# Optimization experiments

Measured on AMD Instinct MI355X. Metric: run time of the kernel, lower is better.

The kernel has to match this reference:

```python
import jax, jax.numpy as jnp
import numpy as np

NUM_CLASSES = 81
NEG_POS_RATIO = 3  # neg_pos init arg
POS_FRAC = 0.02    # realistic fraction of matched (positive) priors


def setup_inputs() -> dict:
    key = jax.random.key(0)
    k1, k2, k3, k4, k5 = jax.random.split(key, 5)
    B, P, C = 32, 24564, NUM_CLASSES
    loc_data = jax.random.normal(k1, (B, P, 4), jnp.float32)
    conf_data = jax.random.normal(k2, (B, P, C), jnp.float32)
    loc_targets = jax.random.normal(k3, (B, P, 4), jnp.float32)
    raw_labels = jax.random.randint(k4, (B, P), 1, C)
    is_pos = jax.random.uniform(k5, (B, P)) < POS_FRAC
    conf_targets = jnp.where(is_pos, raw_labels, 0).astype(jnp.int32)
    return {"loc_data": loc_data, "conf_data": conf_data,
            "loc_targets": loc_targets, "conf_targets": conf_targets}


def _smooth_l1(x):
    ax = jnp.abs(x)
    return jnp.where(ax < 1.0, 0.5 * x * x, ax - 0.5)


def reference(loc_data, conf_data, loc_targets, conf_targets):
    # loc_data [B,P,4], conf_data [B,P,C], conf_targets [B,P] int
    B, P, C = conf_data.shape
    pos = conf_targets > 0  # [B,P]

    # localization smooth-L1 over positive priors only (sum reduction)
    loc_loss = jnp.sum(_smooth_l1(loc_data - loc_targets) * pos[..., None].astype(loc_data.dtype))

    # per-prior CE loss: logsumexp - logit[target]
    lse = jax.nn.logsumexp(conf_data, axis=-1)  # [B,P]
    tgt_logit = jnp.take_along_axis(conf_data, conf_targets[..., None].astype(jnp.int32), axis=-1)[..., 0]
    ce = lse - tgt_logit  # [B,P]

    # hard negative mining: zero out positives, sort descending, pick pivot at 3*num_pos
    mined = jnp.where(pos, 0.0, ce)
    sorted_desc = jnp.flip(jnp.sort(mined, axis=1), axis=1)  # [B,P]
    num_pos = jnp.sum(pos, axis=1)  # [B]
    num_neg = jnp.clip(NEG_POS_RATIO * num_pos, 0, P - 1)
    pivot = jnp.take_along_axis(sorted_desc, num_neg[:, None], axis=1)  # [B,1]
    neg = mined > pivot

    sel = (pos | neg).astype(ce.dtype)
    conf_loss = jnp.sum(ce * sel)

    n_matched = jnp.maximum(jnp.sum(num_pos), 1).astype(conf_data.dtype)
    return (loc_loss + conf_loss) / n_matched
```

## Files before the change

kernel.cpp:

```cpp
#include <hip/hip_runtime.h>
#include <cmath>
#include <cstdint>

#define NB 32
#define NP 24564
#define NC 81
#define NEG_POS 3

static constexpr size_t MINED_ELEMS = (size_t)NB * NP;
static constexpr size_t MINED_BYTES = MINED_ELEMS * sizeof(float);

#define NTILES4 ((int)(MINED_ELEMS / 4))
#define MAIN_BLOCKS 2047
#define TOTAL_WAVES (MAIN_BLOCKS * 4)
#define ITERS 24


__device__ __forceinline__ float wave_reduce_sum(float v) {
#pragma unroll
  for (int off = 32; off > 0; off >>= 1) v += __shfl_down(v, off, 64);
  return v;
}

__device__ __forceinline__ float smooth_l1_4(float4 a, float4 t) {
  float acc = 0.f, d, ax;
  d = a.x - t.x; ax = fabsf(d); acc += (ax < 1.f) ? 0.5f * d * d : ax - 0.5f;
  d = a.y - t.y; ax = fabsf(d); acc += (ax < 1.f) ? 0.5f * d * d : ax - 0.5f;
  d = a.z - t.z; ax = fabsf(d); acc += (ax < 1.f) ? 0.5f * d * d : ax - 0.5f;
  d = a.w - t.w; ax = fabsf(d); acc += (ax < 1.f) ? 0.5f * d * d : ax - 0.5f;
  return acc;
}

__global__ void mb_init(double* __restrict__ acc, int* __restrict__ num_pos) {
  int t = threadIdx.x;
  if (t < 3) acc[t] = 0.0;
  if (t < NB) num_pos[t] = 0;
}

__global__ __launch_bounds__(256, 8) void mb_main(
    const float* __restrict__ conf_data, const int* __restrict__ conf_targets,
    float* __restrict__ mined) {
  __shared__ float lds[4][332];

  const int tid  = (int)threadIdx.x;
  const int wid  = tid >> 6, lane = tid & 63;
  const int r    = lane >> 4, il = lane & 15;
  float* __restrict__ L = lds[wid];

  const int l17   = (lane < 17) ? lane : 16;
  const int ldst1 = (lane < 17) ? (256 + 4 * l17) : 328;

  int tile = (int)blockIdx.x * 4 + wid;
  float4 c0, c1;
  {
    const float4* __restrict__ src =
        reinterpret_cast<const float4*>(conf_data) + (size_t)tile * 81;
    c0 = src[lane];
    c1 = src[64 + l17];
  }

#pragma unroll 1
  for (int k = 0; k < ITERS; ++k) {
    *reinterpret_cast<float4*>(&L[4 * lane]) = c0;
    *reinterpret_cast<float4*>(&L[ldst1]) = c1;

    {
      int nt = tile + TOTAL_WAVES;
      nt = (nt < NTILES4) ? nt : tile;
      const float4* __restrict__ src =
          reinterpret_cast<const float4*>(conf_data) + (size_t)nt * 81;
      c0 = src[lane];
      c1 = src[64 + l17];
    }
    __builtin_amdgcn_sched_barrier(0);

    const int4 tg = *reinterpret_cast<const int4*>(conf_targets + (size_t)tile * 4);
    const int tgt = (r == 0) ? tg.x : (r == 1) ? tg.y : (r == 2) ? tg.z : tg.w;

    const int rb = 81 * r;
    float e = __expf(L[rb + il]) + __expf(L[rb + il + 16]) +
              __expf(L[rb + il + 32]) + __expf(L[rb + il + 48]) +
              __expf(L[rb + il + 64]);
    if (il == 0) e += __expf(L[rb + 80]);
    e += __shfl_xor(e, 1, 64);
    e += __shfl_xor(e, 2, 64);
    e += __shfl_xor(e, 4, 64);
    e += __shfl_xor(e, 8, 64);

    const float tv = L[rb + tgt];
    const float ce = __logf(e) - tv;
    const float val = (tgt > 0) ? -ce : ce;
    mined[tile * 4 + r] = val;

    tile += TOTAL_WAVES;
  }
}

__global__ __launch_bounds__(1024) void mb_select(
    const float* __restrict__ mined, const float* __restrict__ loc_data,
    const float* __restrict__ loc_targets, double* __restrict__ acc,
    int* __restrict__ num_pos) {
  const int b = blockIdx.x;
  const float* __restrict__ row = mined + (size_t)b * NP;
  const int tid = threadIdx.x;
  const int wid = tid >> 6;
  const int lane = tid & 63;

  __shared__ int hist[16][256];
  __shared__ int total[256];
  __shared__ int suffix[256];
  __shared__ unsigned s_prefix;
  __shared__ int s_k;
  __shared__ int s_np;

  {
    int np = 0;
    float cp = 0.f, lv = 0.f;
    for (int q = tid; q < NP / 4; q += 1024) {
      const float4 v = reinterpret_cast<const float4*>(row)[q];
      const float vv[4] = {v.x, v.y, v.z, v.w};
#pragma unroll
      for (int j = 0; j < 4; ++j) {
        if (__float_as_uint(vv[j]) >> 31) {
          np++;
          cp += -vv[j];
          const size_t flat = (size_t)b * NP + 4 * q + j;
          lv += smooth_l1_4(
              *reinterpret_cast<const float4*>(loc_data + flat * 4),
              *reinterpret_cast<const float4*>(loc_targets + flat * 4));
        }
      }
    }
    __shared__ float rednp[16], redcp[16], redlv[16];
    float wnp = wave_reduce_sum((float)np);
    float wcp = wave_reduce_sum(cp);
    float wlv = wave_reduce_sum(lv);
    if (lane == 0) { rednp[wid] = wnp; redcp[wid] = wcp; redlv[wid] = wlv; }
    __syncthreads();
    if (tid == 0) {
      float tnp = 0.f, tcp = 0.f, tlv = 0.f;
#pragma unroll
      for (int i = 0; i < 16; ++i) { tnp += rednp[i]; tcp += redcp[i]; tlv += redlv[i]; }
      const int npi = (int)tnp;
      s_np = npi;
      num_pos[b] = npi;
      if (tcp != 0.f) atomicAdd(&acc[1], (double)tcp);
      if (tlv != 0.f) atomicAdd(&acc[0], (double)tlv);
      int k = NEG_POS * npi;
      if (k > NP - 1) k = NP - 1;
      s_k = k;
      s_prefix = 0u;
    }
    __syncthreads();
  }

  for (int shift = 24; shift >= 0; shift -= 8) {
    for (int i = tid; i < 16 * 256; i += 1024) ((int*)hist)[i] = 0;
    __syncthreads();
    const unsigned mask = (shift == 24) ? 0u : (0xFFFFFFFFu << (shift + 8));
    const unsigned pfx = s_prefix;
    const int kcur = s_k;

    for (int q = tid; q < NP / 4; q += 1024) {
      const float4 v = reinterpret_cast<const float4*>(row)[q];
      unsigned u;
      u = __float_as_uint(v.x); u = (u >> 31) ? 0u : u; if ((u & mask) == pfx) atomicAdd(&hist[wid][(u >> shift) & 255], 1);
      u = __float_as_uint(v.y); u = (u >> 31) ? 0u : u; if ((u & mask) == pfx) atomicAdd(&hist[wid][(u >> shift) & 255], 1);
      u = __float_as_uint(v.z); u = (u >> 31) ? 0u : u; if ((u & mask) == pfx) atomicAdd(&hist[wid][(u >> shift) & 255], 1);
      u = __float_as_uint(v.w); u = (u >> 31) ? 0u : u; if ((u & mask) == pfx) atomicAdd(&hist[wid][(u >> shift) & 255], 1);
    }
    __syncthreads();

    if (tid < 256) {
      int t = 0;
#pragma unroll
      for (int w = 0; w < 16; ++w) t += hist[w][tid];
      total[tid] = t;
    }
    __syncthreads();

    if (wid == 0) {
      const int t0_ = total[4 * lane + 0];
      const int t1_ = total[4 * lane + 1];
      const int t2_ = total[4 * lane + 2];
      const int t3_ = total[4 * lane + 3];
      const int s3 = t3_;
      const int s2 = t2_ + s3;
      const int s1 = t1_ + s2;
      const int s0 = t0_ + s1;
      int acc_ = s0;
#pragma unroll
      for (int off = 1; off < 64; off <<= 1) {
        const int o = __shfl_down(acc_, off, 64);
        if (lane + off < 64) acc_ += o;
      }
      const int excl = acc_ - s0;
      suffix[4 * lane + 0] = s0 + excl;
      suffix[4 * lane + 1] = s1 + excl;
      suffix[4 * lane + 2] = s2 + excl;
      suffix[4 * lane + 3] = s3 + excl;
    }
    __syncthreads();

    if (tid < 256) {
      const int cs = suffix[tid] - total[tid];
      if (kcur >= cs && kcur < cs + total[tid]) {
        s_prefix = pfx | ((unsigned)tid << shift);
        s_k = kcur - cs;
      }
    }
    __syncthreads();
  }

  const unsigned vbits = s_prefix;
  float sum = 0.f;
  for (int q = tid; q < NP / 4; q += 1024) {
    const float4 v = reinterpret_cast<const float4*>(row)[q];
    unsigned u;
    u = __float_as_uint(v.x); u = (u >> 31) ? 0u : u; if (u > vbits) sum += v.x;
    u = __float_as_uint(v.y); u = (u >> 31) ? 0u : u; if (u > vbits) sum += v.y;
    u = __float_as_uint(v.z); u = (u >> 31) ? 0u : u; if (u > vbits) sum += v.z;
    u = __float_as_uint(v.w); u = (u >> 31) ? 0u : u; if (u > vbits) sum += v.w;
  }

  __shared__ float wsum[16];
  float w = wave_reduce_sum(sum);
  if (lane == 0) wsum[wid] = w;
  __syncthreads();
  if (tid == 0) {
    float t = 0.f;
#pragma unroll
    for (int i = 0; i < 16; ++i) t += wsum[i];
    atomicAdd(&acc[2], (double)t);
  }
}

__global__ void mb_finalize(const double* __restrict__ acc,
                            const int* __restrict__ num_pos,
                            float* __restrict__ out) {
  if (threadIdx.x == 0) {
    int tot = 0;
#pragma unroll
    for (int i = 0; i < NB; ++i) tot += num_pos[i];
    const double n = (double)(tot > 0 ? tot : 1);
    out[0] = (float)((acc[0] + acc[1] + acc[2]) / n);
  }
}

extern "C" void kernel_launch(void* const* d_in, const int* in_sizes, int n_in,
                              void* d_out, int out_size, void* d_ws, size_t ws_size,
                              hipStream_t stream) {
  const float* loc_data     = (const float*)d_in[0];
  const float* conf_data    = (const float*)d_in[1];
  const float* loc_targets  = (const float*)d_in[2];
  const int*   conf_targets = (const int*)d_in[3];
  float* out = (float*)d_out;

  float*  mined   = (float*)d_ws;
  double* acc     = (double*)((char*)d_ws + MINED_BYTES);
  int*    num_pos = (int*)((char*)d_ws + MINED_BYTES + 3 * sizeof(double));

  mb_init<<<1, 64, 0, stream>>>(acc, num_pos);

  mb_main<<<MAIN_BLOCKS, 256, 0, stream>>>(conf_data, conf_targets, mined);

  mb_select<<<NB, 1024, 0, stream>>>(mined, loc_data, loc_targets, acc, num_pos);

  mb_finalize<<<1, 64, 0, stream>>>(acc, num_pos, out);
}
```

Measured before the change: 103.6 us.

## Fuse radix-select sum pass into histogram passes, double-buffer main loads, drop init kernel

mb_select now builds the first radix histogram during the positive-count/loc-loss pass and keeps per-bucket float sums, so the sum of negatives above the pivot comes out of the suffix scans. This removes one full histogram pass and the final summation pass over each row. mb_main gets a two-deep register double buffer for conf_data and target loads, which raises memory-level parallelism at some register cost. Per-batch partials are written instead of double atomics, so the mb_init launch is gone. The float LDS atomics and float accumulation order may shift numerics slightly.

```diff
diff --git a/kernel.cpp b/kernel.cpp
--- a/kernel.cpp
+++ b/kernel.cpp
@@ -13,7 +13,7 @@
 #define NTILES4 ((int)(MINED_ELEMS / 4))
 #define MAIN_BLOCKS 2047
 #define TOTAL_WAVES (MAIN_BLOCKS * 4)
-#define ITERS 24
+#define KITERS 12
 
 
 __device__ __forceinline__ float wave_reduce_sum(float v) {
@@ -31,12 +31,6 @@
   return acc;
 }
 
-__global__ void mb_init(double* __restrict__ acc, int* __restrict__ num_pos) {
-  int t = threadIdx.x;
-  if (t < 3) acc[t] = 0.0;
-  if (t < NB) num_pos[t] = 0;
-}
-
 __global__ __launch_bounds__(256, 8) void mb_main(
     const float* __restrict__ conf_data, const int* __restrict__ conf_targets,
     float* __restrict__ mined) {
@@ -50,55 +44,85 @@
   const int l17   = (lane < 17) ? lane : 16;
   const int ldst1 = (lane < 17) ? (256 + 4 * l17) : 328;
 
+#define LOAD_DATA(c0, c1, t)                                            \
+  do {                                                                  \
+    const float4* __restrict__ _s =                                     \
+        reinterpret_cast<const float4*>(conf_data) + (size_t)(t) * 81;  \
+    (c0) = _s[lane];                                                    \
+    (c1) = _s[64 + l17];                                                \
+  } while (0)
+
+#define STAGE(c0, c1)                                     \
+  do {                                                    \
+    *reinterpret_cast<float4*>(&L[4 * lane]) = (c0);      \
+    *reinterpret_cast<float4*>(&L[ldst1]) = (c1);         \
+  } while (0)
+
+#define COMPUTE(t, tg)                                                        \
+  do {                                                                        \
+    const int tgt = (r == 0) ? (tg).x : (r == 1) ? (tg).y                     \
+                  : (r == 2) ? (tg).z : (tg).w;                               \
+    const int rb = 81 * r;                                                    \
+    float e = __expf(L[rb + il]) + __expf(L[rb + il + 16]) +                  \
+              __expf(L[rb + il + 32]) + __expf(L[rb + il + 48]) +             \
+              __expf(L[rb + il + 64]);                                        \
+    if (il == 0) e += __expf(L[rb + 80]);                                     \
+    e += __shfl_xor(e, 1, 64);                                                \
+    e += __shfl_xor(e, 2, 64);                                                \
+    e += __shfl_xor(e, 4, 64);                                                \
+    e += __shfl_xor(e, 8, 64);                                                \
+    const float tv = L[rb + tgt];                                             \
+    const float ce = __logf(e) - tv;                                          \
+    const float val = (tgt > 0) ? -ce : ce;                                   \
+    mined[(t) * 4 + r] = val;                                                 \
+  } while (0)
+
   int tile = (int)blockIdx.x * 4 + wid;
-  float4 c0, c1;
+  float4 a0, a1, b0, b1;
+  int4 tgA, tgB, tgN;
+
+  LOAD_DATA(a0, a1, tile);
+  tgA = *reinterpret_cast<const int4*>(conf_targets + (size_t)tile * 4);
   {
-    const float4* __restrict__ src =
-        reinterpret_cast<const float4*>(conf_data) + (size_t)tile * 81;
-    c0 = src[lane];
-    c1 = src[64 + l17];
+    const int tB = tile + TOTAL_WAVES;
+    LOAD_DATA(b0, b1, tB);
+    tgB = *reinterpret_cast<const int4*>(conf_targets + (size_t)tB * 4);
   }
 
 #pragma unroll 1
-  for (int k = 0; k < ITERS; ++k) {
-    *reinterpret_cast<float4*>(&L[4 * lane]) = c0;
-    *reinterpret_cast<float4*>(&L[ldst1]) = c1;
-
+  for (int k = 0; k < KITERS; ++k) {
+    STAGE(a0, a1);
     {
-      int nt = tile + TOTAL_WAVES;
-      nt = (nt < NTILES4) ? nt : tile;
-      const float4* __restrict__ src =
-          reinterpret_cast<const float4*>(conf_data) + (size_t)nt * 81;
-      c0 = src[lane];
-      c1 = src[64 + l17];
+      int tn = tile + 2 * TOTAL_WAVES;
+      tn = (tn < NTILES4) ? tn : tile;
+      LOAD_DATA(a0, a1, tn);
+      tgN = *reinterpret_cast<const int4*>(conf_targets + (size_t)tn * 4);
     }
     __builtin_amdgcn_sched_barrier(0);
-
-    const int4 tg = *reinterpret_cast<const int4*>(conf_targets + (size_t)tile * 4);
-    const int tgt = (r == 0) ? tg.x : (r == 1) ? tg.y : (r == 2) ? tg.z : tg.w;
-
-    const int rb = 81 * r;
-    float e = __expf(L[rb + il]) + __expf(L[rb + il + 16]) +
-              __expf(L[rb + il + 32]) + __expf(L[rb + il + 48]) +
-              __expf(L[rb + il + 64]);
-    if (il == 0) e += __expf(L[rb + 80]);
-    e += __shfl_xor(e, 1, 64);
-    e += __shfl_xor(e, 2, 64);
-    e += __shfl_xor(e, 4, 64);
-    e += __shfl_xor(e, 8, 64);
-
-    const float tv = L[rb + tgt];
-    const float ce = __logf(e) - tv;
-    const float val = (tgt > 0) ? -ce : ce;
-    mined[tile * 4 + r] = val;
-
+    COMPUTE(tile, tgA);
+    tgA = tgN;
     tile += TOTAL_WAVES;
-  }
+
+    STAGE(b0, b1);
+    {
+      int tn = tile + 2 * TOTAL_WAVES;
+      tn = (tn < NTILES4) ? tn : tile;
+      LOAD_DATA(b0, b1, tn);
+      tgN = *reinterpret_cast<const int4*>(conf_targets + (size_t)tn * 4);
+    }
+    __builtin_amdgcn_sched_barrier(0);
+    COMPUTE(tile, tgB);
+    tgB = tgN;
+    tile += TOTAL_WAVES;
+  }
+#undef LOAD_DATA
+#undef STAGE
+#undef COMPUTE
 }
 
 __global__ __launch_bounds__(1024) void mb_select(
     const float* __restrict__ mined, const float* __restrict__ loc_data,
-    const float* __restrict__ loc_targets, double* __restrict__ acc,
+    const float* __restrict__ loc_targets, float* __restrict__ partial,
     int* __restrict__ num_pos) {
   const int b = blockIdx.x;
   const float* __restrict__ row = mined + (size_t)b * NP;
@@ -106,144 +130,153 @@
   const int wid = tid >> 6;
   const int lane = tid & 63;
 
-  __shared__ int hist[16][256];
-  __shared__ int total[256];
-  __shared__ int suffix[256];
+  __shared__ int   hist[16][256];
+  __shared__ float fsum[16][256];
+  __shared__ int   total[256];
+  __shared__ float ftotal[256];
+  __shared__ int   suffix[256];
+  __shared__ float fsuffix[256];
+  __shared__ float redf[3][16];
   __shared__ unsigned s_prefix;
   __shared__ int s_k;
-  __shared__ int s_np;
+  __shared__ float s_gsum, s_cp, s_lv;
+
+  if (tid == 0) { s_prefix = 0u; s_gsum = 0.f; }
+
+  for (int i = tid; i < 16 * 256; i += 1024) { ((int*)hist)[i] = 0; ((float*)fsum)[i] = 0.f; }
+  __syncthreads();
 
   {
-    int np = 0;
-    float cp = 0.f, lv = 0.f;
+    float np = 0.f, cp = 0.f, lv = 0.f;
     for (int q = tid; q < NP / 4; q += 1024) {
       const float4 v = reinterpret_cast<const float4*>(row)[q];
       const float vv[4] = {v.x, v.y, v.z, v.w};
 #pragma unroll
       for (int j = 0; j < 4; ++j) {
-        if (__float_as_uint(vv[j]) >> 31) {
-          np++;
+        unsigned u = __float_as_uint(vv[j]);
+        if (u >> 31) {
+          np += 1.f;
           cp += -vv[j];
           const size_t flat = (size_t)b * NP + 4 * q + j;
           lv += smooth_l1_4(
               *reinterpret_cast<const float4*>(loc_data + flat * 4),
               *reinterpret_cast<const float4*>(loc_targets + flat * 4));
+          u = 0u;
         }
+        atomicAdd(&hist[wid][u >> 24], 1);
+        atomicAdd(&fsum[wid][u >> 24], __uint_as_float(u));
       }
     }
-    __shared__ float rednp[16], redcp[16], redlv[16];
-    float wnp = wave_reduce_sum((float)np);
+    float wnp = wave_reduce_sum(np);
     float wcp = wave_reduce_sum(cp);
     float wlv = wave_reduce_sum(lv);
-    if (lane == 0) { rednp[wid] = wnp; redcp[wid] = wcp; redlv[wid] = wlv; }
+    if (lane == 0) { redf[0][wid] = wnp; redf[1][wid] = wcp; redf[2][wid] = wlv; }
+  }
+  __syncthreads();
+  if (tid == 0) {
+    float tnp = 0.f, tcp = 0.f, tlv = 0.f;
+#pragma unroll
+    for (int i = 0; i < 16; ++i) { tnp += redf[0][i]; tcp += redf[1][i]; tlv += redf[2][i]; }
+    const int npi = (int)tnp;
+    num_pos[b] = npi;
+    s_cp = tcp; s_lv = tlv;
+    int k = NEG_POS * npi;
+    if (k > NP - 1) k = NP - 1;
+    s_k = k;
+  }
+  __syncthreads();
+
+#define PASS_EPILOGUE(SHIFT)                                                  \
+  do {                                                                        \
+    if (tid < 256) {                                                          \
+      int t = 0; float f = 0.f;                                               \
+      _Pragma("unroll")                                                       \
+      for (int w = 0; w < 16; ++w) { t += hist[w][tid]; f += fsum[w][tid]; }  \
+      total[tid] = t; ftotal[tid] = f;                                        \
+    }                                                                         \
+    __syncthreads();                                                          \
+    if (wid == 0) {                                                           \
+      int t3 = total[4 * lane + 3], t2 = total[4 * lane + 2];                 \
+      int t1 = total[4 * lane + 1], t0 = total[4 * lane + 0];                 \
+      float f3 = ftotal[4 * lane + 3], f2 = ftotal[4 * lane + 2];             \
+      float f1 = ftotal[4 * lane + 1], f0 = ftotal[4 * lane + 0];             \
+      const int is3 = t3, is2 = t2 + is3, is1 = t1 + is2, is0 = t0 + is1;     \
+      const float fs3 = f3, fs2 = f2 + fs3, fs1 = f1 + fs2, fs0 = f0 + fs1;   \
+      int ia = is0; float fa = fs0;                                           \
+      _Pragma("unroll")                                                       \
+      for (int off = 1; off < 64; off <<= 1) {                                \
+        const int io = __shfl_down(ia, off, 64);                              \
+        const float fo = __shfl_down(fa, off, 64);                            \
+        if (lane + off < 64) { ia += io; fa += fo; }                          \
+      }                                                                       \
+      const int iex = ia - is0; const float fex = fa - fs0;                   \
+      suffix[4 * lane + 0] = is0 + iex; fsuffix[4 * lane + 0] = fs0 + fex;    \
+      suffix[4 * lane + 1] = is1 + iex; fsuffix[4 * lane + 1] = fs1 + fex;    \
+      suffix[4 * lane + 2] = is2 + iex; fsuffix[4 * lane + 2] = fs2 + fex;    \
+      suffix[4 * lane + 3] = is3 + iex; fsuffix[4 * lane + 3] = fs3 + fex;    \
+    }                                                                         \
+    __syncthreads();                                                          \
+    if (tid < 256) {                                                          \
+      const int kcur = s_k;                                                   \
+      const int cs = suffix[tid] - total[tid];                                \
+      if (kcur >= cs && kcur < cs + total[tid]) {                             \
+        s_prefix |= ((unsigned)tid << (SHIFT));                               \
+        s_k = kcur - cs;                                                      \
+        s_gsum += fsuffix[tid] - ftotal[tid];                                 \
+      }                                                                       \
+    }                                                                         \
+    __syncthreads();                                                          \
+  } while (0)
+
+  PASS_EPILOGUE(24);
+
+  for (int shift = 16; shift >= 0; shift -= 8) {
+    for (int i = tid; i < 16 * 256; i += 1024) { ((int*)hist)[i] = 0; ((float*)fsum)[i] = 0.f; }
     __syncthreads();
-    if (tid == 0) {
-      float tnp = 0.f, tcp = 0.f, tlv = 0.f;
-#pragma unroll
-      for (int i = 0; i < 16; ++i) { tnp += rednp[i]; tcp += redcp[i]; tlv += redlv[i]; }
-      const int npi = (int)tnp;
-      s_np = npi;
-      num_pos[b] = npi;
-      if (tcp != 0.f) atomicAdd(&acc[1], (double)tcp);
-      if (tlv != 0.f) atomicAdd(&acc[0], (double)tlv);
-      int k = NEG_POS * npi;
-      if (k > NP - 1) k = NP - 1;
-      s_k = k;
-      s_prefix = 0u;
-    }
-    __syncthreads();
-  }
-
-  for (int shift = 24; shift >= 0; shift -= 8) {
-    for (int i = tid; i < 16 * 256; i += 1024) ((int*)hist)[i] = 0;
-    __syncthreads();
-    const unsigned mask = (shift == 24) ? 0u : (0xFFFFFFFFu << (shift + 8));
+    const unsigned mask = 0xFFFFFFFFu << (shift + 8);
     const unsigned pfx = s_prefix;
-    const int kcur = s_k;
 
     for (int q = tid; q < NP / 4; q += 1024) {
       const float4 v = reinterpret_cast<const float4*>(row)[q];
       unsigned u;
-      u = __float_as_uint(v.x); u = (u >> 31) ? 0u : u; if ((u & mask) == pfx) atomicAdd(&hist[wid][(u >> shift) & 255], 1);
-      u = __float_as_uint(v.y); u = (u >> 31) ? 0u : u; if ((u & mask) == pfx) atomicAdd(&hist[wid][(u >> shift) & 255], 1);
-      u = __float_as_uint(v.z); u = (u >> 31) ? 0u : u; if ((u & mask) == pfx) atomicAdd(&hist[wid][(u >> shift) & 255], 1);
-      u = __float_as_uint(v.w); u = (u >> 31) ? 0u : u; if ((u & mask) == pfx) atomicAdd(&hist[wid][(u >> shift) & 255], 1);
+      u = __float_as_uint(v.x); u = (u >> 31) ? 0u : u;
+      if ((u & mask) == pfx) { atomicAdd(&hist[wid][(u >> shift) & 255], 1); atomicAdd(&fsum[wid][(u >> shift) & 255], __uint_as_float(u)); }
+      u = __float_as_uint(v.y); u = (u >> 31) ? 0u : u;
+      if ((u & mask) == pfx) { atomicAdd(&hist[wid][(u >> shift) & 255], 1); atomicAdd(&fsum[wid][(u >> shift) & 255], __uint_as_float(u)); }
+      u = __float_as_uint(v.z); u = (u >> 31) ? 0u : u;
+      if ((u & mask) == pfx) { atomicAdd(&hist[wid][(u >> shift) & 255], 1); atomicAdd(&fsum[wid][(u >> shift) & 255], __uint_as_float(u)); }
+      u = __float_as_uint(v.w); u = (u >> 31) ? 0u : u;
+      if ((u & mask) == pfx) { atomicAdd(&hist[wid][(u >> shift) & 255], 1); atomicAdd(&fsum[wid][(u >> shift) & 255], __uint_as_float(u)); }
     }
     __syncthreads();
 
-    if (tid < 256) {
-      int t = 0;
-#pragma unroll
-      for (int w = 0; w < 16; ++w) t += hist[w][tid];
-      total[tid] = t;
-    }
-    __syncthreads();
-
-    if (wid == 0) {
-      const int t0_ = total[4 * lane + 0];
-      const int t1_ = total[4 * lane + 1];
-      const int t2_ = total[4 * lane + 2];
-      const int t3_ = total[4 * lane + 3];
-      const int s3 = t3_;
-      const int s2 = t2_ + s3;
-      const int s1 = t1_ + s2;
-      const int s0 = t0_ + s1;
-      int acc_ = s0;
-#pragma unroll
-      for (int off = 1; off < 64; off <<= 1) {
-        const int o = __shfl_down(acc_, off, 64);
-        if (lane + off < 64) acc_ += o;
-      }
-      const int excl = acc_ - s0;
-      suffix[4 * lane + 0] = s0 + excl;
-      suffix[4 * lane + 1] = s1 + excl;
-      suffix[4 * lane + 2] = s2 + excl;
-      suffix[4 * lane + 3] = s3 + excl;
-    }
-    __syncthreads();
-
-    if (tid < 256) {
-      const int cs = suffix[tid] - total[tid];
-      if (kcur >= cs && kcur < cs + total[tid]) {
-        s_prefix = pfx | ((unsigned)tid << shift);
-        s_k = kcur - cs;
-      }
-    }
-    __syncthreads();
-  }
-
-  const unsigned vbits = s_prefix;
-  float sum = 0.f;
-  for (int q = tid; q < NP / 4; q += 1024) {
-    const float4 v = reinterpret_cast<const float4*>(row)[q];
-    unsigned u;
-    u = __float_as_uint(v.x); u = (u >> 31) ? 0u : u; if (u > vbits) sum += v.x;
-    u = __float_as_uint(v.y); u = (u >> 31) ? 0u : u; if (u > vbits) sum += v.y;
-    u = __float_as_uint(v.z); u = (u >> 31) ? 0u : u; if (u > vbits) sum += v.z;
-    u = __float_as_uint(v.w); u = (u >> 31) ? 0u : u; if (u > vbits) sum += v.w;
-  }
-
-  __shared__ float wsum[16];
-  float w = wave_reduce_sum(sum);
-  if (lane == 0) wsum[wid] = w;
-  __syncthreads();
+    if (shift == 16) PASS_EPILOGUE(16);
+    else if (shift == 8) PASS_EPILOGUE(8);
+    else PASS_EPILOGUE(0);
+  }
+#undef PASS_EPILOGUE
+
   if (tid == 0) {
-    float t = 0.f;
-#pragma unroll
-    for (int i = 0; i < 16; ++i) t += wsum[i];
-    atomicAdd(&acc[2], (double)t);
-  }
-}
-
-__global__ void mb_finalize(const double* __restrict__ acc,
+    partial[b * 4 + 0] = s_lv;
+    partial[b * 4 + 1] = s_cp;
+    partial[b * 4 + 2] = s_gsum;
+  }
+}
+
+__global__ void mb_finalize(const float* __restrict__ partial,
                             const int* __restrict__ num_pos,
                             float* __restrict__ out) {
   if (threadIdx.x == 0) {
+    double s = 0.0;
     int tot = 0;
 #pragma unroll
-    for (int i = 0; i < NB; ++i) tot += num_pos[i];
+    for (int i = 0; i < NB; ++i) {
+      s += (double)partial[i * 4 + 0] + (double)partial[i * 4 + 1] +
+           (double)partial[i * 4 + 2];
+      tot += num_pos[i];
+    }
     const double n = (double)(tot > 0 ? tot : 1);
-    out[0] = (float)((acc[0] + acc[1] + acc[2]) / n);
+    out[0] = (float)(s / n);
   }
 }
 
@@ -256,15 +289,13 @@
   const int*   conf_targets = (const int*)d_in[3];
   float* out = (float*)d_out;
 
-  float*  mined   = (float*)d_ws;
-  double* acc     = (double*)((char*)d_ws + MINED_BYTES);
-  int*    num_pos = (int*)((char*)d_ws + MINED_BYTES + 3 * sizeof(double));
-
-  mb_init<<<1, 64, 0, stream>>>(acc, num_pos);
+  float* mined   = (float*)d_ws;
+  float* partial = (float*)((char*)d_ws + MINED_BYTES);
+  int*   num_pos = (int*)((char*)d_ws + MINED_BYTES + 512);
 
   mb_main<<<MAIN_BLOCKS, 256, 0, stream>>>(conf_data, conf_targets, mined);
 
-  mb_select<<<NB, 1024, 0, stream>>>(mined, loc_data, loc_targets, acc, num_pos);
-
-  mb_finalize<<<1, 64, 0, stream>>>(acc, num_pos, out);
-}
+  mb_select<<<NB, 1024, 0, stream>>>(mined, loc_data, loc_targets, partial, num_pos);
+
+  mb_finalize<<<1, 64, 0, stream>>>(partial, num_pos, out);
+}
```

Measured after the change: 151.3 us. 1.46x slower.
